# Kernel tuning notes

Measured on AMD Instinct MI355X. Metric: run time of the kernel, lower is better.

Reference implementation:

```python
import jax, jax.numpy as jnp
import numpy as np
import math

INF = 1e12  # constant.INFINITY_NUMBER in the original repo


def setup_inputs() -> dict:
    key = jax.random.key(0)
    ks = jax.random.split(key, 12)
    B, S, W, D = 16, 512, 8, 768
    M, Wm = 2, 64
    U, Wu = 32, 16
    V = 32000
    words = jax.random.randint(ks[0], (B, S, W), 0, V)
    masks = jax.random.randint(ks[1], (B, S, W), 0, 2).astype(bool)
    main = jax.random.randint(ks[2], (B, M, Wm), 0, V)
    main_mask = jax.random.randint(ks[3], (B, M, Wm), 0, 2).astype(bool)
    user = jax.random.randint(ks[4], (B, U, Wu), 0, V)
    user_mask = jax.random.randint(ks[5], (B, U, Wu), 0, 2).astype(bool)
    # sparse-ish dependency adjacency
    adj = (jax.random.uniform(ks[6], (B, S, S)) < 0.05).astype(jnp.float32)
    emb_weight = jax.random.normal(ks[7], (V, D), jnp.float32) * 0.02
    K_w = jax.random.normal(ks[8], (D, D), jnp.float32) * (1.0 / math.sqrt(D))
    K_b = jnp.zeros((D,), jnp.float32)
    Q_w = jax.random.normal(ks[9], (D, D), jnp.float32) * (1.0 / math.sqrt(D))
    Q_b = jnp.zeros((D,), jnp.float32)
    return {"words": words, "masks": masks, "main": main, "main_mask": main_mask,
            "user": user, "user_mask": user_mask, "adj": adj,
            "emb_weight": emb_weight, "K_w": K_w, "K_b": K_b, "Q_w": Q_w, "Q_b": Q_b}


def _masked_max(embs, mask, axis):
    # masked_fill(mask, -INF) -> max(axis) ; caller fixes residual -INF rows
    return jnp.max(jnp.where(mask[..., None], -INF, embs), axis=axis)


def reference(words, masks, main, main_mask, user, user_mask, adj,
              emb_weight, K_w, K_b, Q_w, Q_b):
    D = emb_weight.shape[1]

    word_embs = emb_weight[words]   # [B,S,W,D]
    main_embs = emb_weight[main]    # [B,M,Wm,D]
    user_embs = emb_weight[user]    # [B,U,Wu,D]

    # node mask from adjacency: True where node has no in/out edges
    mask = ((adj.sum(axis=2) + adj.sum(axis=1)) == 0)[:, :, None]  # [B,S,1]

    # main: masked max-pool over word pieces, zero fully-masked rows
    main_e = _masked_max(main_embs, main_mask, axis=2)             # [B,M,D]
    main_e = jnp.where(main_e == -INF, 0.0, main_e)

    # user: masked max-pool over word pieces then over users
    user_e = _masked_max(user_embs, user_mask, axis=2)             # [B,U,D]
    user_e = jnp.max(user_e, axis=1)                               # [B,D]
    user_e = jnp.where(user_e == -INF, 0.0, user_e)

    # token embeddings: masked max-pool over word pieces (no -INF fix in original)
    g = _masked_max(word_embs, masks, axis=2)                      # [B,S,D]

    # single-head attention: softmax(K g (Q g)^T / sqrt(D)) @ g
    key_ = g @ K_w.T + K_b                                         # [B,S,D]
    query = g @ Q_w.T + Q_b                                        # [B,S,D]
    scores = jnp.einsum('bsd,btd->bst', key_, query) / math.sqrt(D)
    dense_graph = jax.nn.softmax(scores, axis=2)                   # [B,S,S]
    gcn_out = jnp.einsum('bst,btd->bsd', dense_graph, g)           # [B,S,D]

    adj_sm = jax.nn.softmax(adj, axis=2)

    return (gcn_out, mask, dense_graph, adj_sm,
            jnp.squeeze(main_e), jnp.squeeze(user_e))
```

## Files before the change

kernel.cpp:

```cpp
#include <hip/hip_runtime.h>
#include <hip/hip_bf16.h>
#include <math.h>

static constexpr int Bn = 16, Sn = 512, Wn = 8, Dn = 768;
static constexpr int Mn_ = 2, WMn = 64;
static constexpr int Un = 32, WUn = 16;

#define INF_VAL 1e12f
#define INV_SQRT_D 0.03608439182435161f

static constexpr size_t OFF_GCN   = 0;
static constexpr size_t OFF_MASK  = 6291456;
static constexpr size_t OFF_DENSE = 6299648;
static constexpr size_t OFF_ADJ   = 10493952;
static constexpr size_t OFF_MAIN  = 14688256;
static constexpr size_t OFF_USER  = 14712832;

static constexpr size_t WSB_GBF     = 0;
static constexpr size_t WSB_GT      = 12582912;
static constexpr size_t WSB_DENSEBF = 25165824;
static constexpr size_t WSB_HBF     = 33554432;
static constexpr size_t WSB_KWT     = 46137344;
static constexpr size_t WSB_QWT     = 47316992;
static constexpr size_t WSB_MT      = 48496640;
static constexpr size_t WSB_PARTU   = 49676288;
static constexpr size_t WSB_PARTM   = 51249152;
static constexpr size_t WSB_KBAR    = 51642368;
static constexpr size_t WSB_QBAR    = 51648512;
static constexpr size_t WSB_U       = 51654656;
static constexpr size_t WSB_V       = 51660800;
static constexpr size_t WSB_VA      = 51666944;
static constexpr size_t WSB_VB      = 51673088;
static constexpr size_t WSB_CONSTS  = 51679232;
static constexpr size_t WSB_QS      = 51679296;
static constexpr size_t WSB_KQ      = 51712064;
static constexpr size_t WSB_GA      = 51744832;
static constexpr size_t WSB_GB      = 51777600;
static constexpr size_t WSB_COLSUM  = 51810368;
static constexpr size_t WSB_FLAGS   = 51843136;
static constexpr size_t WSB_ROWSUM  = 51875904;
static constexpr size_t WSB_UVU     = 51908672;
static constexpr size_t WSB_UVV     = 51957824;
static constexpr size_t WSB_UVA     = 52006976;
static constexpr size_t WSB_UVB     = 52056128;

typedef __attribute__((ext_vector_type(8))) short short8;
typedef __attribute__((ext_vector_type(4))) float f32x4;

static __device__ __forceinline__ ushort f2bf(float f) {
    union { float f; unsigned u; } v; v.f = f;
    unsigned u = v.u;
    unsigned r = (u + 0x7FFFu + ((u >> 16) & 1u)) >> 16;
    return (ushort)r;
}

static __device__ __forceinline__ void gload16(const void* g, void* lds) {
    __builtin_amdgcn_global_load_lds(
        (const __attribute__((address_space(1))) void*)g,
        (__attribute__((address_space(3))) void*)lds, 16, 0, 0);
}

static __device__ __forceinline__ void fmax4(float4& a, const float4& x) {
    a.x = fmaxf(a.x, x.x); a.y = fmaxf(a.y, x.y);
    a.z = fmaxf(a.z, x.z); a.w = fmaxf(a.w, x.w);
}

__global__ __launch_bounds__(256)
void fold1(const float* __restrict__ K_w, const float* __restrict__ K_b,
           const float* __restrict__ Q_w, const float* __restrict__ Q_b,
           double* __restrict__ kbar, double* __restrict__ qbar,
           ushort* __restrict__ KwbT, ushort* __restrict__ QwbT,
           float* __restrict__ colsum) {
    int blk = blockIdx.x, t = threadIdx.x;
    if (blk < 192) {
        int wv = t >> 6, lane = t & 63;
        int r = blk * 4 + wv;
        double sk = 0.0, sq = 0.0;
        for (int d = lane; d < Dn; d += 64) {
            sk += (double)K_w[(size_t)r * Dn + d];
            sq += (double)Q_w[(size_t)r * Dn + d];
        }
        #pragma unroll
        for (int off = 32; off > 0; off >>= 1) {
            sk += __shfl_down(sk, off, 64);
            sq += __shfl_down(sq, off, 64);
        }
        if (lane == 0) {
            kbar[r] = -1e12 * sk + (double)K_b[r];
            qbar[r] = -1e12 * sq + (double)Q_b[r];
        }
    } else if (blk < 1344) {
        int tt = blk - 192;
        const float* src = (tt < 576) ? K_w : Q_w;
        ushort* dst = (tt < 576) ? KwbT : QwbT;
        int t6 = (tt < 576) ? tt : tt - 576;
        int e0 = (t6 % 24) * 32, i0 = (t6 / 24) * 32;
        __shared__ ushort tile[32][33];
        int tx = t & 31, ty = t >> 5;
        #pragma unroll
        for (int i2 = 0; i2 < 4; ++i2)
            tile[ty + i2 * 8][tx] = f2bf(src[(size_t)(e0 + ty + i2 * 8) * Dn + i0 + tx]);
        __syncthreads();
        #pragma unroll
        for (int i2 = 0; i2 < 4; ++i2)
            dst[(size_t)(i0 + ty + i2 * 8) * Dn + e0 + tx] = tile[tx][ty + i2 * 8];
    } else {
        for (int i = t; i < Bn * Sn; i += 256) colsum[i] = 0.f;
    }
}

__global__ __launch_bounds__(64)
void uv_part(const float* __restrict__ K_w, const float* __restrict__ Q_w,
             const float* __restrict__ K_b, const float* __restrict__ Q_b,
             const double* __restrict__ kbar, const double* __restrict__ qbar,
             double* __restrict__ uvu, double* __restrict__ uvv,
             double* __restrict__ uva, double* __restrict__ uvb) {
    int j = blockIdx.x * 64 + threadIdx.x;
    int e0 = blockIdx.y * 96;
    double su = 0.0, sv = 0.0, sa = 0.0, sb = 0.0;
    for (int e = e0; e < e0 + 96; ++e) {
        double kw = (double)K_w[(size_t)e * Dn + j];
        double qw = (double)Q_w[(size_t)e * Dn + j];
        su += kw * qbar[e];
        sv += qw * kbar[e];
        sa += kw * (double)Q_b[e];
        sb += qw * (double)K_b[e];
    }
    uvu[(size_t)blockIdx.y * Dn + j] = su;
    uvv[(size_t)blockIdx.y * Dn + j] = sv;
    uva[(size_t)blockIdx.y * Dn + j] = sa;
    uvb[(size_t)blockIdx.y * Dn + j] = sb;
}

__global__ __launch_bounds__(64)
void uvred_consts(const double* __restrict__ uvu, const double* __restrict__ uvv,
                  const double* __restrict__ uva, const double* __restrict__ uvb,
                  const double* __restrict__ kbar, const double* __restrict__ qbar,
                  const float* __restrict__ K_b, const float* __restrict__ Q_b,
                  double* __restrict__ u, double* __restrict__ v,
                  double* __restrict__ va, double* __restrict__ vb,
                  double* __restrict__ consts) {
    int blk = blockIdx.x;
    int l = threadIdx.x;
    if (blk < 12) {
        int j = blk * 64 + l;
        double su = 0.0, sv = 0.0, sa = 0.0, sb = 0.0;
        #pragma unroll
        for (int c = 0; c < 8; ++c) {
            su += uvu[(size_t)c * Dn + j];
            sv += uvv[(size_t)c * Dn + j];
            sa += uva[(size_t)c * Dn + j];
            sb += uvb[(size_t)c * Dn + j];
        }
        u[j] = su; v[j] = sv; va[j] = sa; vb[j] = sb;
    } else {
        double c0 = 0.0, c1 = 0.0, c2 = 0.0, c3 = 0.0;
        for (int e = l; e < Dn; e += 64) {
            c0 += kbar[e] * (double)Q_b[e];
            c1 += kbar[e] * qbar[e];
            c2 += qbar[e] * (double)K_b[e];
            c3 += (double)K_b[e] * (double)Q_b[e];
        }
        #pragma unroll
        for (int off = 32; off > 0; off >>= 1) {
            c0 += __shfl_down(c0, off, 64);
            c1 += __shfl_down(c1, off, 64);
            c2 += __shfl_down(c2, off, 64);
            c3 += __shfl_down(c3, off, 64);
        }
        if (l == 0) { consts[0] = c0; consts[1] = c1; consts[2] = c2; consts[3] = c3; }
    }
}

__global__ __launch_bounds__(512)
void adjsm_colsum_kernel(const float* __restrict__ adj, float* __restrict__ adjsm,
                         float* __restrict__ colsum, float* __restrict__ rowsum) {
    int blk = blockIdx.x;
    int b = blk >> 5, rc = blk & 31;
    int t = threadIdx.x;
    const float* base = adj + ((size_t)b * Sn + rc * 16) * Sn;
    float* obase = adjsm + ((size_t)b * Sn + rc * 16) * Sn;
    const float EM1 = 0.36787944117144233f;
    const float EP1 = 2.718281828459045f;
    __shared__ float red[8];
    float colacc = 0.f;
    for (int r = 0; r < 16; ++r) {
        float a = base[(size_t)r * Sn + t];
        colacc += a;
        float s = a;
        #pragma unroll
        for (int off = 32; off > 0; off >>= 1) s += __shfl_down(s, off, 64);
        if ((t & 63) == 0) red[t >> 6] = s;
        __syncthreads();
        float n1 = red[0] + red[1] + red[2] + red[3]
                 + red[4] + red[5] + red[6] + red[7];
        float e1, e0;
        if (n1 > 0.f) { e1 = 1.f; e0 = EM1; } else { e1 = EP1; e0 = 1.f; }
        float denom = n1 * e1 + (512.f - n1) * e0;
        float inv = 1.f / denom;
        obase[(size_t)r * Sn + t] = (a == 1.f ? e1 : e0) * inv;
        if (t == 0) rowsum[(size_t)b * Sn + rc * 16 + r] = n1;
        __syncthreads();
    }
    atomicAdd(&colsum[(size_t)b * Sn + t], colacc);
}

__global__ __launch_bounds__(192)
void pool_g_s1(const int* __restrict__ words, const int* __restrict__ masks,
               const int* __restrict__ main_idx, const int* __restrict__ mmask,
               const int* __restrict__ user_idx, const int* __restrict__ umask,
               const float* __restrict__ emb,
               const double* __restrict__ u, const double* __restrict__ v,
               const double* __restrict__ va, const double* __restrict__ vb,
               const double* __restrict__ consts,
               ushort* __restrict__ gbf, float* __restrict__ qs,
               float* __restrict__ kq, float* __restrict__ ga,
               float* __restrict__ gb, int* __restrict__ flags,
               float* __restrict__ partM, float* __restrict__ partU) {
    int blk = blockIdx.x;
    int t = threadIdx.x;
    if (blk >= Bn * Sn) {
        int s1 = blk - Bn * Sn;
        const int *irow, *mrow;
        float* dst;
        if (s1 < 128) {
            int bm = s1 >> 2, ch = s1 & 3;
            irow = main_idx + (size_t)bm * WMn + ch * 16;
            mrow = mmask + (size_t)bm * WMn + ch * 16;
            dst = partM + (size_t)s1 * Dn;
        } else {
            int bu = s1 - 128;
            irow = user_idx + (size_t)bu * WUn;
            mrow = umask + (size_t)bu * WUn;
            dst = partU + (size_t)bu * Dn;
        }
        float4 acc = make_float4(-INF_VAL, -INF_VAL, -INF_VAL, -INF_VAL);
        #pragma unroll
        for (int w = 0; w < 16; ++w) {
            if (mrow[w] != 0) continue;
            float4 x = ((const float4*)(emb + (size_t)irow[w] * Dn))[t];
            fmax4(acc, x);
        }
        ((float4*)dst)[t] = acc;
        return;
    }
    int bs = blk;
    const int* wrow = words + (size_t)bs * Wn;
    const int* mrow = masks + (size_t)bs * Wn;
    float4 acc = make_float4(-INF_VAL, -INF_VAL, -INF_VAL, -INF_VAL);
    int nm = 0;
    #pragma unroll
    for (int w = 0; w < Wn; ++w) {
        int mk = mrow[w];
        nm += (mk != 0);
        if (mk != 0) continue;
        float4 x = ((const float4*)(emb + (size_t)wrow[w] * Dn))[t];
        fmax4(acc, x);
    }
    ushort4 o;
    o.x = f2bf(acc.x); o.y = f2bf(acc.y); o.z = f2bf(acc.z); o.w = f2bf(acc.w);
    ((ushort4*)(gbf + (size_t)bs * Dn))[t] = o;
    int j = t * 4;
    double dv = v[j] * (double)acc.x + v[j+1] * (double)acc.y
              + v[j+2] * (double)acc.z + v[j+3] * (double)acc.w;
    double du = u[j] * (double)acc.x + u[j+1] * (double)acc.y
              + u[j+2] * (double)acc.z + u[j+3] * (double)acc.w;
    double da = va[j] * (double)acc.x + va[j+1] * (double)acc.y
              + va[j+2] * (double)acc.z + va[j+3] * (double)acc.w;
    double db = vb[j] * (double)acc.x + vb[j+1] * (double)acc.y
              + vb[j+2] * (double)acc.z + vb[j+3] * (double)acc.w;
    #pragma unroll
    for (int off = 32; off > 0; off >>= 1) {
        dv += __shfl_down(dv, off, 64);
        du += __shfl_down(du, off, 64);
        da += __shfl_down(da, off, 64);
        db += __shfl_down(db, off, 64);
    }
    __shared__ double rr[12];
    if ((t & 63) == 0) {
        rr[t >> 6] = dv; rr[3 + (t >> 6)] = du;
        rr[6 + (t >> 6)] = da; rr[9 + (t >> 6)] = db;
    }
    __syncthreads();
    if (t == 0) {
        qs[bs] = (float)(rr[0] + rr[1] + rr[2] + consts[0]);
        kq[bs] = (float)(rr[3] + rr[4] + rr[5] + consts[2]);
        ga[bs] = (float)(rr[6] + rr[7] + rr[8]);
        gb[bs] = (float)(rr[9] + rr[10] + rr[11]);
        flags[bs] = (nm == Wn) ? 1 : 0;
    }
}

__global__ __launch_bounds__(192)
void pool_s2m(const float* __restrict__ partM, const float* __restrict__ partU,
              float* __restrict__ outM, float* __restrict__ outU,
              const float* __restrict__ rowsum, const float* __restrict__ colsum,
              float* __restrict__ maskout) {
    int blk = blockIdx.x;
    int t = threadIdx.x;
    if (blk >= 48) {
        int i = (blk - 48) * 192 + t;
        if (i < Bn * Sn)
            maskout[i] = ((rowsum[i] + colsum[i]) == 0.f) ? 1.f : 0.f;
        return;
    }
    float4 acc = make_float4(-INF_VAL, -INF_VAL, -INF_VAL, -INF_VAL);
    float* dst;
    if (blk < 32) {
        #pragma unroll
        for (int c = 0; c < 4; ++c) {
            float4 x = ((const float4*)(partM + (size_t)(blk * 4 + c) * Dn))[t];
            fmax4(acc, x);
        }
        dst = outM + (size_t)blk * Dn;
    } else {
        int b = blk - 32;
        for (int u2 = 0; u2 < Un; ++u2) {
            float4 x = ((const float4*)(partU + (size_t)(b * Un + u2) * Dn))[t];
            fmax4(acc, x);
        }
        dst = outU + (size_t)b * Dn;
    }
    if (acc.x == -INF_VAL) acc.x = 0.f;
    if (acc.y == -INF_VAL) acc.y = 0.f;
    if (acc.z == -INF_VAL) acc.z = 0.f;
    if (acc.w == -INF_VAL) acc.w = 0.f;
    ((float4*)dst)[t] = acc;
}

__global__ __launch_bounds__(256)
void transpose_g(const ushort* __restrict__ gbf, ushort* __restrict__ gT) {
    __shared__ ushort tile[32][33];
    int b = blockIdx.z;
    int d0 = blockIdx.x * 32, s0 = blockIdx.y * 32;
    int tx = threadIdx.x & 31, ty = threadIdx.x >> 5;
    #pragma unroll
    for (int i = 0; i < 4; ++i)
        tile[ty + i * 8][tx] = gbf[((size_t)(b * Sn + s0 + ty + i * 8)) * Dn + d0 + tx];
    __syncthreads();
    #pragma unroll
    for (int i = 0; i < 4; ++i)
        gT[((size_t)(b * Dn + d0 + ty + i * 8)) * Sn + s0 + tx] = tile[tx][ty + i * 8];
}

template<int OUT_BF16, int BN>
__global__ __launch_bounds__(256)
void gemm_mfma(const ushort* __restrict__ A, const ushort* __restrict__ B,
               void* __restrict__ Cout,
               int Km, int lda, int ldb, int ldc,
               long long sA, long long sB, long long sC) {
    constexpr int NFB = BN / 32;
    __shared__ ushort As[128 * 64];
    __shared__ ushort Bs[BN * 64];
    const ushort* Ab = A + (size_t)blockIdx.z * sA;
    const ushort* Bb = B + (size_t)blockIdx.z * sB;
    int i0 = blockIdx.y * 128, j0 = blockIdx.x * BN;
    int tid = threadIdx.x;
    int lane = tid & 63, wv = tid >> 6;
    int wr = wv >> 1, wc = wv & 1;
    int ln15 = lane & 15, lkg = lane >> 4;
    int sub = lane >> 3;
    int c8  = lane & 7;

    f32x4 acc[4][NFB] = {};

    for (int k0 = 0; k0 < Km; k0 += 64) {
        #pragma unroll
        for (int it = 0; it < 4; ++it) {
            int r = it * 32 + wv * 8 + sub;
            int cc = c8 ^ (r & 7);
            ushort* dstA = As + (it * 4096 + wv * 1024) / 2;
            gload16(Ab + (size_t)(i0 + r) * lda + k0 + cc * 8, dstA);
        }
        #pragma unroll
        for (int it = 0; it < BN / 32; ++it) {
            int r = it * 32 + wv * 8 + sub;
            int cc = c8 ^ (r & 7);
            ushort* dstB = Bs + (it * 4096 + wv * 1024) / 2;
            gload16(Bb + (size_t)(j0 + r) * ldb + k0 + cc * 8, dstB);
        }
        __syncthreads();
        #pragma unroll
        for (int kh = 0; kh < 2; ++kh) {
            short8 af[4], bfr[NFB];
            int kc = kh * 4 + lkg;
            #pragma unroll
            for (int f = 0; f < 4; ++f) {
                int ra = wr * 64 + f * 16 + ln15;
                af[f] = *(const short8*)((const char*)As + ra * 128 + ((kc ^ (ra & 7)) << 4));
            }
            #pragma unroll
            for (int f = 0; f < NFB; ++f) {
                int rb = wc * (BN / 2) + f * 16 + ln15;
                bfr[f] = *(const short8*)((const char*)Bs + rb * 128 + ((kc ^ (rb & 7)) << 4));
            }
            #pragma unroll
            for (int fa = 0; fa < 4; ++fa)
                #pragma unroll
                for (int fb = 0; fb < NFB; ++fb)
                    acc[fa][fb] = __builtin_amdgcn_mfma_f32_16x16x32_bf16(
                        af[fa], bfr[fb], acc[fa][fb], 0, 0, 0);
        }
        __syncthreads();
    }

    #pragma unroll
    for (int fa = 0; fa < 4; ++fa) {
        #pragma unroll
        for (int fb = 0; fb < NFB; ++fb) {
            int n = j0 + wc * (BN / 2) + fb * 16 + ln15;
            #pragma unroll
            for (int rr = 0; rr < 4; ++rr) {
                int m = i0 + wr * 64 + fa * 16 + lkg * 4 + rr;
                float val = acc[fa][fb][rr];
                if (OUT_BF16) {
                    ((ushort*)Cout)[(size_t)blockIdx.z * sC + (size_t)m * ldc + n] = f2bf(val);
                } else {
                    ((float*)Cout)[(size_t)blockIdx.z * sC + (size_t)m * ldc + n] = val;
                }
            }
        }
    }
}

__global__ __launch_bounds__(256)
void softmax_fix(float* __restrict__ dense, const int* __restrict__ flags,
                 const float* __restrict__ qs, const float* __restrict__ kq,
                 const float* __restrict__ ga, const float* __restrict__ gb,
                 const double* __restrict__ consts, ushort* __restrict__ densebf) {
    int bs = blockIdx.x;
    int b = bs >> 9;
    int t = threadIdx.x;
    float* row = dense + (size_t)bs * 512;
    int f0 = flags[(b << 9) + t];
    int f1 = flags[(b << 9) + t + 256];
    bool sm = flags[bs] != 0;
    float x0, x1;
    if (sm) {
        float c1i = (float)consts[1] * INV_SQRT_D;
        x0 = f0 ? c1i : qs[(b << 9) + t] * INV_SQRT_D;
        x1 = f1 ? c1i : qs[(b << 9) + t + 256] * INV_SQRT_D;
    } else {
        float kqi = kq[bs] * INV_SQRT_D;
        float corr = ga[bs] + (float)consts[3];
        x0 = f0 ? kqi : (row[t] + corr + gb[(b << 9) + t]) * INV_SQRT_D;
        x1 = f1 ? kqi : (row[t + 256] + corr + gb[(b << 9) + t + 256]) * INV_SQRT_D;
    }
    float m = fmaxf(x0, x1);
    #pragma unroll
    for (int off = 32; off > 0; off >>= 1) m = fmaxf(m, __shfl_down(m, off, 64));
    __shared__ float red[4];
    __shared__ float bmax, bsum;
    if ((t & 63) == 0) red[t >> 6] = m;
    __syncthreads();
    if (t == 0) bmax = fmaxf(fmaxf(red[0], red[1]), fmaxf(red[2], red[3]));
    __syncthreads();
    float mx = bmax;
    float e0 = expf(x0 - mx), e1 = expf(x1 - mx);
    float s = e0 + e1;
    #pragma unroll
    for (int off = 32; off > 0; off >>= 1) s += __shfl_down(s, off, 64);
    if ((t & 63) == 0) red[t >> 6] = s;
    __syncthreads();
    if (t == 0) bsum = red[0] + red[1] + red[2] + red[3];
    __syncthreads();
    float inv = 1.f / bsum;
    float p0 = e0 * inv, p1 = e1 * inv;
    row[t] = p0; row[t + 256] = p1;
    ushort* bro = densebf + (size_t)bs * 512;
    bro[t] = f2bf(p0); bro[t + 256] = f2bf(p1);
}

extern "C" void kernel_launch(void* const* d_in, const int* in_sizes, int n_in,
                              void* d_out, int out_size, void* d_ws, size_t ws_size,
                              hipStream_t stream) {
    const int*   words     = (const int*)d_in[0];
    const int*   masks     = (const int*)d_in[1];
    const int*   main_idx  = (const int*)d_in[2];
    const int*   main_mask = (const int*)d_in[3];
    const int*   user_idx  = (const int*)d_in[4];
    const int*   user_mask = (const int*)d_in[5];
    const float* adj       = (const float*)d_in[6];
    const float* emb       = (const float*)d_in[7];
    const float* K_w       = (const float*)d_in[8];
    const float* K_b       = (const float*)d_in[9];
    const float* Q_w       = (const float*)d_in[10];
    const float* Q_b       = (const float*)d_in[11];

    float* out = (float*)d_out;
    char*  ws8 = (char*)d_ws;

    ushort* gbf     = (ushort*)(ws8 + WSB_GBF);
    ushort* gT      = (ushort*)(ws8 + WSB_GT);
    ushort* densebf = (ushort*)(ws8 + WSB_DENSEBF);
    ushort* hbf     = (ushort*)(ws8 + WSB_HBF);
    ushort* KwbT    = (ushort*)(ws8 + WSB_KWT);
    ushort* QwbT    = (ushort*)(ws8 + WSB_QWT);
    ushort* Mt      = (ushort*)(ws8 + WSB_MT);
    float*  partU   = (float*)(ws8 + WSB_PARTU);
    float*  partM   = (float*)(ws8 + WSB_PARTM);
    double* kbar    = (double*)(ws8 + WSB_KBAR);
    double* qbar    = (double*)(ws8 + WSB_QBAR);
    double* u       = (double*)(ws8 + WSB_U);
    double* v       = (double*)(ws8 + WSB_V);
    double* va      = (double*)(ws8 + WSB_VA);
    double* vb      = (double*)(ws8 + WSB_VB);
    double* consts  = (double*)(ws8 + WSB_CONSTS);
    float*  qs      = (float*)(ws8 + WSB_QS);
    float*  kq      = (float*)(ws8 + WSB_KQ);
    float*  ga      = (float*)(ws8 + WSB_GA);
    float*  gb      = (float*)(ws8 + WSB_GB);
    float*  colsum  = (float*)(ws8 + WSB_COLSUM);
    int*    flags   = (int*)(ws8 + WSB_FLAGS);
    float*  rowsum  = (float*)(ws8 + WSB_ROWSUM);
    double* uvu     = (double*)(ws8 + WSB_UVU);
    double* uvv     = (double*)(ws8 + WSB_UVV);
    double* uva     = (double*)(ws8 + WSB_UVA);
    double* uvb     = (double*)(ws8 + WSB_UVB);

    float* dense = out + OFF_DENSE;

    fold1<<<1345, 256, 0, stream>>>(K_w, K_b, Q_w, Q_b, kbar, qbar, KwbT, QwbT, colsum);

    gemm_mfma<1, 64><<<dim3(12, 6, 1), 256, 0, stream>>>(
        QwbT, KwbT, Mt, Dn, Dn, Dn, Dn, 0, 0, 0);

    uv_part<<<dim3(Dn / 64, 8), 64, 0, stream>>>(K_w, Q_w, K_b, Q_b, kbar, qbar,
                                                 uvu, uvv, uva, uvb);
    uvred_consts<<<13, 64, 0, stream>>>(uvu, uvv, uva, uvb, kbar, qbar, K_b, Q_b,
                                        u, v, va, vb, consts);

    adjsm_colsum_kernel<<<Bn * 32, 512, 0, stream>>>(adj, out + OFF_ADJ, colsum, rowsum);

    pool_g_s1<<<Bn * Sn + 640, 192, 0, stream>>>(
        words, masks, main_idx, main_mask, user_idx, user_mask, emb,
        u, v, va, vb, consts, gbf, qs, kq, ga, gb, flags, partM, partU);
    pool_s2m<<<91, 192, 0, stream>>>(partM, partU, out + OFF_MAIN, out + OFF_USER,
                                     rowsum, colsum, out + OFF_MASK);

    transpose_g<<<dim3(Dn / 32, Sn / 32, Bn), 256, 0, stream>>>(gbf, gT);

    gemm_mfma<1, 64><<<dim3(12, 64, 1), 256, 0, stream>>>(
        gbf, Mt, hbf, Dn, Dn, Dn, Dn, 0, 0, 0);

    gemm_mfma<0, 64><<<dim3(8, 4, Bn), 256, 0, stream>>>(
        hbf, gbf, dense, Dn, Dn, Dn, Sn,
        (long long)Sn * Dn, (long long)Sn * Dn, (long long)Sn * Sn);

    softmax_fix<<<Bn * Sn, 256, 0, stream>>>(dense, flags, qs, kq, ga, gb, consts, densebf);

    gemm_mfma<0, 64><<<dim3(12, 4, Bn), 256, 0, stream>>>(
        densebf, gT, out + OFF_GCN, Sn, Sn, Sn, Dn,
        (long long)Sn * Sn, (long long)Dn * Sn, (long long)Sn * Dn);
}
```

Before: 164.9 us.

## Merge small launches and deepen GEMM K-tile to 128

The uv partial-sum work is folded into the adjacency softmax kernel as extra blocks, and the g transpose is merged with the main/user pooling reduction and mask output into one mid kernel. This cuts kernel launch count and the tail gaps between small kernels. The GEMM now stages 128-wide K slices with a 16-way XOR swizzle, halving barrier iterations, but it doubles LDS use per block (48KB), which may lower occupancy. The weight-product GEMM is also moved after uvred.

Measured after the change: 157.3 us. -4.6%, faster.

```diff
diff --git a/kernel.cpp b/kernel.cpp
--- a/kernel.cpp
+++ b/kernel.cpp
@@ -109,27 +109,62 @@
     }
 }
 
-__global__ __launch_bounds__(64)
-void uv_part(const float* __restrict__ K_w, const float* __restrict__ Q_w,
-             const float* __restrict__ K_b, const float* __restrict__ Q_b,
-             const double* __restrict__ kbar, const double* __restrict__ qbar,
-             double* __restrict__ uvu, double* __restrict__ uvv,
-             double* __restrict__ uva, double* __restrict__ uvb) {
-    int j = blockIdx.x * 64 + threadIdx.x;
-    int e0 = blockIdx.y * 96;
-    double su = 0.0, sv = 0.0, sa = 0.0, sb = 0.0;
-    for (int e = e0; e < e0 + 96; ++e) {
-        double kw = (double)K_w[(size_t)e * Dn + j];
-        double qw = (double)Q_w[(size_t)e * Dn + j];
-        su += kw * qbar[e];
-        sv += qw * kbar[e];
-        sa += kw * (double)Q_b[e];
-        sb += qw * (double)K_b[e];
-    }
-    uvu[(size_t)blockIdx.y * Dn + j] = su;
-    uvv[(size_t)blockIdx.y * Dn + j] = sv;
-    uva[(size_t)blockIdx.y * Dn + j] = sa;
-    uvb[(size_t)blockIdx.y * Dn + j] = sb;
+__global__ __launch_bounds__(512)
+void adjsm_uv_kernel(const float* __restrict__ adj, float* __restrict__ adjsm,
+                     float* __restrict__ colsum, float* __restrict__ rowsum,
+                     const float* __restrict__ K_w, const float* __restrict__ Q_w,
+                     const float* __restrict__ K_b, const float* __restrict__ Q_b,
+                     const double* __restrict__ kbar, const double* __restrict__ qbar,
+                     double* __restrict__ uvu, double* __restrict__ uvv,
+                     double* __restrict__ uva, double* __restrict__ uvb) {
+    int blk = blockIdx.x;
+    int t = threadIdx.x;
+    if (blk >= 512) {
+        int id = (blk - 512) * 512 + t;
+        int c = id / 768;
+        int j = id - c * 768;
+        int e0 = c * 96;
+        double su = 0.0, sv = 0.0, sa = 0.0, sb = 0.0;
+        for (int e = e0; e < e0 + 96; ++e) {
+            double kw = (double)K_w[(size_t)e * Dn + j];
+            double qw = (double)Q_w[(size_t)e * Dn + j];
+            su += kw * qbar[e];
+            sv += qw * kbar[e];
+            sa += kw * (double)Q_b[e];
+            sb += qw * (double)K_b[e];
+        }
+        uvu[(size_t)c * Dn + j] = su;
+        uvv[(size_t)c * Dn + j] = sv;
+        uva[(size_t)c * Dn + j] = sa;
+        uvb[(size_t)c * Dn + j] = sb;
+        return;
+    }
+    int b = blk >> 5, rc = blk & 31;
+    const float* base = adj + ((size_t)b * Sn + rc * 16) * Sn;
+    float* obase = adjsm + ((size_t)b * Sn + rc * 16) * Sn;
+    const float EM1 = 0.36787944117144233f;
+    const float EP1 = 2.718281828459045f;
+    __shared__ float red[8];
+    float colacc = 0.f;
+    for (int r = 0; r < 16; ++r) {
+        float a = base[(size_t)r * Sn + t];
+        colacc += a;
+        float s = a;
+        #pragma unroll
+        for (int off = 32; off > 0; off >>= 1) s += __shfl_down(s, off, 64);
+        if ((t & 63) == 0) red[t >> 6] = s;
+        __syncthreads();
+        float n1 = red[0] + red[1] + red[2] + red[3]
+                 + red[4] + red[5] + red[6] + red[7];
+        float e1, e0;
+        if (n1 > 0.f) { e1 = 1.f; e0 = EM1; } else { e1 = EP1; e0 = 1.f; }
+        float denom = n1 * e1 + (512.f - n1) * e0;
+        float inv = 1.f / denom;
+        obase[(size_t)r * Sn + t] = (a == 1.f ? e1 : e0) * inv;
+        if (t == 0) rowsum[(size_t)b * Sn + rc * 16 + r] = n1;
+        __syncthreads();
+    }
+    atomicAdd(&colsum[(size_t)b * Sn + t], colacc);
 }
 
 __global__ __launch_bounds__(64)
@@ -170,39 +205,6 @@
         }
         if (l == 0) { consts[0] = c0; consts[1] = c1; consts[2] = c2; consts[3] = c3; }
     }
-}
-
-__global__ __launch_bounds__(512)
-void adjsm_colsum_kernel(const float* __restrict__ adj, float* __restrict__ adjsm,
-                         float* __restrict__ colsum, float* __restrict__ rowsum) {
-    int blk = blockIdx.x;
-    int b = blk >> 5, rc = blk & 31;
-    int t = threadIdx.x;
-    const float* base = adj + ((size_t)b * Sn + rc * 16) * Sn;
-    float* obase = adjsm + ((size_t)b * Sn + rc * 16) * Sn;
-    const float EM1 = 0.36787944117144233f;
-    const float EP1 = 2.718281828459045f;
-    __shared__ float red[8];
-    float colacc = 0.f;
-    for (int r = 0; r < 16; ++r) {
-        float a = base[(size_t)r * Sn + t];
-        colacc += a;
-        float s = a;
-        #pragma unroll
-        for (int off = 32; off > 0; off >>= 1) s += __shfl_down(s, off, 64);
-        if ((t & 63) == 0) red[t >> 6] = s;
-        __syncthreads();
-        float n1 = red[0] + red[1] + red[2] + red[3]
-                 + red[4] + red[5] + red[6] + red[7];
-        float e1, e0;
-        if (n1 > 0.f) { e1 = 1.f; e0 = EM1; } else { e1 = EP1; e0 = 1.f; }
-        float denom = n1 * e1 + (512.f - n1) * e0;
-        float inv = 1.f / denom;
-        obase[(size_t)r * Sn + t] = (a == 1.f ? e1 : e0) * inv;
-        if (t == 0) rowsum[(size_t)b * Sn + rc * 16 + r] = n1;
-        __syncthreads();
-    }
-    atomicAdd(&colsum[(size_t)b * Sn + t], colacc);
 }
 
 __global__ __launch_bounds__(192)
@@ -291,30 +293,48 @@
     }
 }
 
-__global__ __launch_bounds__(192)
-void pool_s2m(const float* __restrict__ partM, const float* __restrict__ partU,
-              float* __restrict__ outM, float* __restrict__ outU,
-              const float* __restrict__ rowsum, const float* __restrict__ colsum,
-              float* __restrict__ maskout) {
+__global__ __launch_bounds__(256)
+void mid_kernel(const ushort* __restrict__ gbf, ushort* __restrict__ gT,
+                const float* __restrict__ partM, const float* __restrict__ partU,
+                float* __restrict__ outM, float* __restrict__ outU,
+                const float* __restrict__ rowsum, const float* __restrict__ colsum,
+                float* __restrict__ maskout) {
     int blk = blockIdx.x;
     int t = threadIdx.x;
-    if (blk >= 48) {
-        int i = (blk - 48) * 192 + t;
+    if (blk < 6144) {
+        __shared__ ushort tile[32][33];
+        int b = blk / 384;
+        int rem = blk - b * 384;
+        int d0 = (rem % 24) * 32, s0 = (rem / 24) * 32;
+        int tx = t & 31, ty = t >> 5;
+        #pragma unroll
+        for (int i = 0; i < 4; ++i)
+            tile[ty + i * 8][tx] = gbf[((size_t)(b * Sn + s0 + ty + i * 8)) * Dn + d0 + tx];
+        __syncthreads();
+        #pragma unroll
+        for (int i = 0; i < 4; ++i)
+            gT[((size_t)(b * Dn + d0 + ty + i * 8)) * Sn + s0 + tx] = tile[tx][ty + i * 8];
+        return;
+    }
+    if (blk >= 6192) {
+        int i = (blk - 6192) * 256 + t;
         if (i < Bn * Sn)
             maskout[i] = ((rowsum[i] + colsum[i]) == 0.f) ? 1.f : 0.f;
         return;
     }
+    if (t >= 192) return;
     float4 acc = make_float4(-INF_VAL, -INF_VAL, -INF_VAL, -INF_VAL);
     float* dst;
-    if (blk < 32) {
+    if (blk < 6176) {
+        int bm = blk - 6144;
         #pragma unroll
         for (int c = 0; c < 4; ++c) {
-            float4 x = ((const float4*)(partM + (size_t)(blk * 4 + c) * Dn))[t];
+            float4 x = ((const float4*)(partM + (size_t)(bm * 4 + c) * Dn))[t];
             fmax4(acc, x);
         }
-        dst = outM + (size_t)blk * Dn;
+        dst = outM + (size_t)bm * Dn;
     } else {
-        int b = blk - 32;
+        int b = blk - 6176;
         for (int u2 = 0; u2 < Un; ++u2) {
             float4 x = ((const float4*)(partU + (size_t)(b * Un + u2) * Dn))[t];
             fmax4(acc, x);
@@ -328,76 +348,60 @@
     ((float4*)dst)[t] = acc;
 }
 
-__global__ __launch_bounds__(256)
-void transpose_g(const ushort* __restrict__ gbf, ushort* __restrict__ gT) {
-    __shared__ ushort tile[32][33];
-    int b = blockIdx.z;
-    int d0 = blockIdx.x * 32, s0 = blockIdx.y * 32;
-    int tx = threadIdx.x & 31, ty = threadIdx.x >> 5;
-    #pragma unroll
-    for (int i = 0; i < 4; ++i)
-        tile[ty + i * 8][tx] = gbf[((size_t)(b * Sn + s0 + ty + i * 8)) * Dn + d0 + tx];
-    __syncthreads();
-    #pragma unroll
-    for (int i = 0; i < 4; ++i)
-        gT[((size_t)(b * Dn + d0 + ty + i * 8)) * Sn + s0 + tx] = tile[tx][ty + i * 8];
-}
-
-template<int OUT_BF16, int BN>
+template<int OUT_BF16>
 __global__ __launch_bounds__(256)
 void gemm_mfma(const ushort* __restrict__ A, const ushort* __restrict__ B,
                void* __restrict__ Cout,
                int Km, int lda, int ldb, int ldc,
                long long sA, long long sB, long long sC) {
-    constexpr int NFB = BN / 32;
-    __shared__ ushort As[128 * 64];
-    __shared__ ushort Bs[BN * 64];
+    __shared__ ushort As[128 * 128];
+    __shared__ ushort Bs[64 * 128];
     const ushort* Ab = A + (size_t)blockIdx.z * sA;
     const ushort* Bb = B + (size_t)blockIdx.z * sB;
-    int i0 = blockIdx.y * 128, j0 = blockIdx.x * BN;
+    int i0 = blockIdx.y * 128, j0 = blockIdx.x * 64;
     int tid = threadIdx.x;
     int lane = tid & 63, wv = tid >> 6;
     int wr = wv >> 1, wc = wv & 1;
     int ln15 = lane & 15, lkg = lane >> 4;
-    int sub = lane >> 3;
-    int c8  = lane & 7;
-
-    f32x4 acc[4][NFB] = {};
-
-    for (int k0 = 0; k0 < Km; k0 += 64) {
-        #pragma unroll
-        for (int it = 0; it < 4; ++it) {
-            int r = it * 32 + wv * 8 + sub;
-            int cc = c8 ^ (r & 7);
+    int r4 = lane >> 4;
+    int c16 = lane & 15;
+
+    f32x4 acc[4][2] = {};
+
+    for (int k0 = 0; k0 < Km; k0 += 128) {
+        #pragma unroll
+        for (int it = 0; it < 8; ++it) {
+            int r = it * 16 + wv * 4 + r4;
+            int cc = c16 ^ (r & 15);
             ushort* dstA = As + (it * 4096 + wv * 1024) / 2;
             gload16(Ab + (size_t)(i0 + r) * lda + k0 + cc * 8, dstA);
         }
         #pragma unroll
-        for (int it = 0; it < BN / 32; ++it) {
-            int r = it * 32 + wv * 8 + sub;
-            int cc = c8 ^ (r & 7);
+        for (int it = 0; it < 4; ++it) {
+            int r = it * 16 + wv * 4 + r4;
+            int cc = c16 ^ (r & 15);
             ushort* dstB = Bs + (it * 4096 + wv * 1024) / 2;
             gload16(Bb + (size_t)(j0 + r) * ldb + k0 + cc * 8, dstB);
         }
         __syncthreads();
         #pragma unroll
-        for (int kh = 0; kh < 2; ++kh) {
-            short8 af[4], bfr[NFB];
+        for (int kh = 0; kh < 4; ++kh) {
+            short8 af[4], bfr[2];
             int kc = kh * 4 + lkg;
             #pragma unroll
             for (int f = 0; f < 4; ++f) {
                 int ra = wr * 64 + f * 16 + ln15;
-                af[f] = *(const short8*)((const char*)As + ra * 128 + ((kc ^ (ra & 7)) << 4));
+                af[f] = *(const short8*)((const char*)As + ra * 256 + ((kc ^ (ra & 15)) << 4));
             }
             #pragma unroll
-            for (int f = 0; f < NFB; ++f) {
-                int rb = wc * (BN / 2) + f * 16 + ln15;
-                bfr[f] = *(const short8*)((const char*)Bs + rb * 128 + ((kc ^ (rb & 7)) << 4));
+            for (int f = 0; f < 2; ++f) {
+                int rb = wc * 32 + f * 16 + ln15;
+                bfr[f] = *(const short8*)((const char*)Bs + rb * 256 + ((kc ^ (rb & 15)) << 4));
             }
             #pragma unroll
             for (int fa = 0; fa < 4; ++fa)
                 #pragma unroll
-                for (int fb = 0; fb < NFB; ++fb)
+                for (int fb = 0; fb < 2; ++fb)
                     acc[fa][fb] = __builtin_amdgcn_mfma_f32_16x16x32_bf16(
                         af[fa], bfr[fb], acc[fa][fb], 0, 0, 0);
         }
@@ -407,8 +411,8 @@
     #pragma unroll
     for (int fa = 0; fa < 4; ++fa) {
         #pragma unroll
-        for (int fb = 0; fb < NFB; ++fb) {
-            int n = j0 + wc * (BN / 2) + fb * 16 + ln15;
+        for (int fb = 0; fb < 2; ++fb) {
+            int n = j0 + wc * 32 + fb * 16 + ln15;
             #pragma unroll
             for (int rr = 0; rr < 4; ++rr) {
                 int m = i0 + wr * 64 + fa * 16 + lkg * 4 + rr;
@@ -522,34 +526,34 @@
 
     fold1<<<1345, 256, 0, stream>>>(K_w, K_b, Q_w, Q_b, kbar, qbar, KwbT, QwbT, colsum);
 
-    gemm_mfma<1, 64><<<dim3(12, 6, 1), 256, 0, stream>>>(
-        QwbT, KwbT, Mt, Dn, Dn, Dn, Dn, 0, 0, 0);
-
-    uv_part<<<dim3(Dn / 64, 8), 64, 0, stream>>>(K_w, Q_w, K_b, Q_b, kbar, qbar,
-                                                 uvu, uvv, uva, uvb);
+    adjsm_uv_kernel<<<524, 512, 0, stream>>>(adj, out + OFF_ADJ, colsum, rowsum,
+                                             K_w, Q_w, K_b, Q_b, kbar, qbar,
+                                             uvu, uvv, uva, uvb);
+
     uvred_consts<<<13, 64, 0, stream>>>(uvu, uvv, uva, uvb, kbar, qbar, K_b, Q_b,
                                         u, v, va, vb, consts);
 
-    adjsm_colsum_kernel<<<Bn * 32, 512, 0, stream>>>(adj, out + OFF_ADJ, colsum, rowsum);
+    gemm_mfma<1><<<dim3(12, 6, 1), 256, 0, stream>>>(
+        QwbT, KwbT, Mt, Dn, Dn, Dn, Dn, 0, 0, 0);
 
     pool_g_s1<<<Bn * Sn + 640, 192, 0, stream>>>(
         words, masks, main_idx, main_mask, user_idx, user_mask, emb,
         u, v, va, vb, consts, gbf, qs, kq, ga, gb, flags, partM, partU);
-    pool_s2m<<<91, 192, 0, stream>>>(partM, partU, out + OFF_MAIN, out + OFF_USER,
-                                     rowsum, colsum, out + OFF_MASK);
-
-    transpose_g<<<dim3(Dn / 32, Sn / 32, Bn), 256, 0, stream>>>(gbf, gT);
-
-    gemm_mfma<1, 64><<<dim3(12, 64, 1), 256, 0, stream>>>(
+
+    mid_kernel<<<6224, 256, 0, stream>>>(gbf, gT, partM, partU,
+                                         out + OFF_MAIN, out + OFF_USER,
+                                         rowsum, colsum, out + OFF_MASK);
+
+    gemm_mfma<1><<<dim3(12, 64, 1), 256, 0, stream>>>(
         gbf, Mt, hbf, Dn, Dn, Dn, Dn, 0, 0, 0);
 
-    gemm_mfma<0, 64><<<dim3(8, 4, Bn), 256, 0, stream>>>(
+    gemm_mfma<0><<<dim3(8, 4, Bn), 256, 0, stream>>>(
         hbf, gbf, dense, Dn, Dn, Dn, Sn,
         (long long)Sn * Dn, (long long)Sn * Dn, (long long)Sn * Sn);
 
     softmax_fix<<<Bn * Sn, 256, 0, stream>>>(dense, flags, qs, kq, ga, gb, consts, densebf);
 
-    gemm_mfma<0, 64><<<dim3(12, 4, Bn), 256, 0, stream>>>(
+    gemm_mfma<0><<<dim3(12, 4, Bn), 256, 0, stream>>>(
         densebf, gT, out + OFF_GCN, Sn, Sn, Sn, Dn,
         (long long)Sn * Sn, (long long)Dn * Sn, (long long)Sn * Dn);
 }
```
